# Kernel optimization log

Measured on AMD Instinct MI355X. Metric: run time of the kernel, lower is better.

Reference implementation:

```python
import jax, jax.numpy as jnp
import numpy as np
from jax import lax

VOX_DIMS = (9, 9, 9)
VOX = 9 * 9 * 9  # 729 voxels per sample


def setup_inputs() -> dict:
    rng = np.random.default_rng(0)
    N, B = 1_000_000, 32
    Cin, Fd, Cout = 3, 64, 64
    # per-point voxel index in the flat batched grid [0, B*VOX)
    voxel = rng.integers(0, B * VOX, size=N)
    unique, inverse = np.unique(voxel, return_inverse=True)

    key = jax.random.key(0)
    ks = jax.random.split(key, 12)
    s = 0.1
    inp = {
        "x": jax.random.normal(ks[0], (N, Cin), jnp.float32),
        "lin0_w": jax.random.normal(ks[1], (Cin, Fd), jnp.float32) * s,
        "lin0_b": jax.random.normal(ks[2], (Fd,), jnp.float32) * s,
        "conv0_w": jax.random.normal(ks[3], (Fd, Cin, 3, 3, 3), jnp.float32) * s,
        "conv0_b": jax.random.normal(ks[4], (Fd,), jnp.float32) * s,
        "lin1_w": jax.random.normal(ks[5], (Fd, Cout), jnp.float32) * s,
        "lin1_b": jax.random.normal(ks[6], (Cout,), jnp.float32) * s,
        "conv1_w": jax.random.normal(ks[7], (Cout, Fd, 3, 3, 3), jnp.float32) * s,
        "conv1_b": jax.random.normal(ks[8], (Cout,), jnp.float32) * s,
        "linf_w": jax.random.normal(ks[9], (Cin, Cout), jnp.float32) * s,
        "linf_b": jax.random.normal(ks[10], (Cout,), jnp.float32) * s,
        "consecutive_cluster": jnp.asarray(inverse, jnp.int32),
        "cluster_non_consecutive": jnp.asarray(voxel, jnp.int32),
        "unique_cluster_non_consecutive": jnp.asarray(unique, jnp.int32),
        "batch_size": B,
    }
    return inp


def _elm(x, lin_w, lin_b, conv_w, conv_b, consec, cnc, unc, B):
    """One EquivariantLinearMapsModule forward (use_attention is forced False)."""
    Cin = x.shape[1]
    Cout = lin_w.shape[1]
    inner = x @ lin_w + lin_b  # [N, Cout]

    U = unc.shape[0]
    sums = jax.ops.segment_sum(x, consec, num_segments=U)           # [U, Cin]
    counts = jax.ops.segment_sum(jnp.ones((x.shape[0], 1), x.dtype), consec, num_segments=U)
    means = sums / counts                                           # scatter_mean

    # grid[:, unique] = means.T ; then raw view to (B, Cin, 9, 9, 9) as in torch
    grid = jnp.zeros((Cin, B * VOX), x.dtype).at[:, unc].set(means.T)
    grid = grid.reshape((B, Cin) + VOX_DIMS)
    out = lax.conv_general_dilated(
        grid, conv_w, window_strides=(1, 1, 1), padding=[(1, 1)] * 3,
        dimension_numbers=("NCDHW", "OIDHW", "NCDHW"))
    out = out + conv_b[None, :, None, None, None]
    # raw view back to (Cout, B*VOX) then gather per point
    outer = out.reshape(Cout, -1)[:, cnc].T  # [N, Cout]
    return inner + outer


def reference(x, lin0_w, lin0_b, conv0_w, conv0_b, lin1_w, lin1_b, conv1_w, conv1_b,
              linf_w, linf_b, consecutive_cluster, cluster_non_consecutive,
              unique_cluster_non_consecutive, batch_size):
    x0 = x
    h = _elm(x0, lin0_w, lin0_b, conv0_w, conv0_b,
             consecutive_cluster, cluster_non_consecutive,
             unique_cluster_non_consecutive, batch_size)
    h = _elm(h, lin1_w, lin1_b, conv1_w, conv1_b,
             consecutive_cluster, cluster_non_consecutive,
             unique_cluster_non_consecutive, batch_size)
    # input_nc (3) < output_nc (64): residual via lin_first
    return h + (x0 @ linf_w + linf_b)
```

## Files before the change

### kernel.cpp

```cpp
#include <hip/hip_runtime.h>
#include <hip/hip_bf16.h>
#include <stdint.h>

typedef __hip_bfloat16 bf16;
typedef _Float16 half_t;
typedef _Float16 half8 __attribute__((ext_vector_type(8)));
typedef float f32x4 __attribute__((ext_vector_type(4)));
typedef unsigned short us8 __attribute__((ext_vector_type(8)));

#define BVOXN 23328

__device__ __forceinline__ float b2f(bf16 v) { return __bfloat162float(v); }

#define OFF_L0W   64
#define OFF_B0    256
#define OFF_W0    320
#define OFF_CB0   5504
#define OFF_CB1   120320
#define OFF_SUMS  120640
#define OFF_GA0   213952
#define OFF_MEX   283936
#define OFF_GT    377248
#define OFF_C0T   1123744
#define OFF_WT    1870240
#define OFF_WC    1927584
#define OFF_BVEC  1927776
#define OFF_G     1927840

#define FP_SCALE 1048576.0f
#define FP_BIAS  8388608

__global__ void k_probe(const void* lin1_w, int* flag) {
    __shared__ int cnt[256];
    int t = threadIdx.x;
    const bf16* p = (const bf16*)lin1_w;
    int c = 0;
    for (int j = t; j < 2048; j += 256) {
        float v = b2f(p[2 * j]);
        if (!(v == v) || fabsf(v) > 64.0f || (v != 0.0f && fabsf(v) < 1e-20f)) c++;
    }
    cnt[t] = c;
    __syncthreads();
    for (int s = 128; s > 0; s >>= 1) {
        if (t < s) cnt[t] += cnt[t + s];
        __syncthreads();
    }
    if (t == 0) *flag = (cnt[0] > 100) ? 1 : 0;
}

__device__ __forceinline__ float ldf(const void* p, int j, int isf) {
    return isf ? ((const float*)p)[j] : b2f(((const bf16*)p)[j]);
}

#define SETUP_N 120256
__global__ void k_sa(const void* x, const int* consec, int N, int NA,
                     const void* l0w, const void* l0b, const void* w0,
                     const void* cb0, const void* l1w, const void* l1b,
                     const void* w1, const void* cb1, const void* lfw,
                     const void* lfb, const int* flag, float* ws,
                     half_t* Wt, float* Wc, float* bvec,
                     unsigned long long* sums8) {
    int isf = *flag;
    int bid = blockIdx.x;
    if (bid < NA) {
        int i = bid * 256 + threadIdx.x;
        if (i >= N) return;
        int u = consec[i];
        float v0 = ldf(x, 3 * i + 0, isf);
        float v1 = ldf(x, 3 * i + 1, isf);
        float v2 = ldf(x, 3 * i + 2, isf);
        unsigned e0 = (unsigned)(__float2int_rn(v0 * FP_SCALE) + FP_BIAS);
        unsigned e1 = (unsigned)(__float2int_rn(v1 * FP_SCALE) + FP_BIAS);
        unsigned e2 = (unsigned)(__float2int_rn(v2 * FP_SCALE) + FP_BIAS);
        atomicAdd(&sums8[2 * u + 0], ((unsigned long long)e0 << 32) | e1);
        atomicAdd(&sums8[2 * u + 1], (1ull << 32) | e2);
        return;
    }
    int t = (bid - NA) * 256 + threadIdx.x;
    if (t < SETUP_N) {
        if (t < 5568) {
            const void* src;
            int j;
            float* dst;
            if (t < 192)       { src = l0w; j = t;         dst = ws + OFF_L0W + j; }
            else if (t < 256)  { src = l0b; j = t - 192;   dst = ws + 256 + (j = t - 192, j); }
            else if (t < 5440) {
                j = t - 256;
                int o = j / 81, r = j % 81, i = r / 27, tap = r % 27;
                src = w0;
                dst = ws + OFF_W0 + (i * 27 + tap) * 64 + o;
            }
            else if (t < 5504) { src = cb0; j = t - 5440;  dst = ws + OFF_CB0 + j; }
            else               { src = cb1; j = t - 5504;  dst = ws + OFF_CB1 + j; }
            if (t >= 192 && t < 256) { src = l0b; j = t - 192; dst = ws + OFF_B0 + j; }
            *dst = ldf(src, j, isf);
        } else {
            int q = t - 5568;
            int tap = q >> 12;
            int r = q & 4095;
            int o = r >> 6, i = r & 63;
            float v;
            if (tap < 27) v = ldf(w1, (o * 64 + i) * 27 + tap, isf);
            else          v = ldf(l1w, i * 64 + o, isf);
            Wt[q] = (half_t)v;
        }
        return;
    }
    if (bid == NA + (SETUP_N + 255) / 256 && threadIdx.x < 64) {
        int c = threadIdx.x;
        float bv = ldf(l1b, c, isf) + ldf(lfb, c, isf);
        for (int k = 0; k < 64; ++k)
            bv += ldf(l0b, k, isf) * ldf(l1w, k * 64 + c, isf);
        bvec[c] = bv;
        for (int r = 0; r < 3; ++r) {
            float wv = ldf(lfw, r * 64 + c, isf);
            for (int k = 0; k < 64; ++k)
                wv += ldf(l0w, r * 64 + k, isf) * ldf(l1w, k * 64 + c, isf);
            Wc[r * 64 + c] = wv;
        }
    }
}

__device__ __forceinline__ void decode_mean(const unsigned long long* sums8, int u,
                                            float& m0, float& m1, float& m2) {
    unsigned long long S1 = sums8[2 * u + 0];
    unsigned long long S2 = sums8[2 * u + 1];
    double n = (double)(unsigned)(S2 >> 32);
    double k = 1.0 / (1048576.0 * n);
    double nb = n * 8388608.0;
    m0 = (float)(((double)(unsigned)(S1 >> 32) - nb) * k);
    m1 = (float)(((double)(unsigned)(S1 & 0xffffffffu) - nb) * k);
    m2 = (float)(((double)(unsigned)(S2 & 0xffffffffu) - nb) * k);
}

__global__ void k_scatter0(const unsigned long long* sums8, const int* unc,
                           float* gridA0, f32x4* meanex, int U) {
    int u = blockIdx.x * 256 + threadIdx.x;
    if (u >= U) return;
    int v = unc[u];
    float m0, m1, m2;
    decode_mean(sums8, u, m0, m1, m2);
    gridA0[0 * BVOXN + v] = m0;
    gridA0[1 * BVOXN + v] = m1;
    gridA0[2 * BVOXN + v] = m2;
    f32x4 m = {m0, m1, m2, 1.0f};
    meanex[v] = m;
}

__global__ __launch_bounds__(256) void k_conv0s(const float* gridA0, const float* w0t,
                                                const float* cb0, half_t* conv0oT) {
    __shared__ float slab[3 * 363];
    int b = blockIdx.x / 9, d = blockIdx.x % 9;
    int t = threadIdx.x;
    for (int s = t; s < 3 * 363; s += 256) {
        int i = s / 363, rr = s % 363;
        int zz = rr / 121, p = rr % 121;
        int ph = p / 11, pw = p % 11;
        int z = d + zz - 1, hh = ph - 1, ww = pw - 1;
        float v = 0.0f;
        if ((unsigned)z < 9u && (unsigned)hh < 9u && (unsigned)ww < 9u)
            v = gridA0[b * 2187 + i * 729 + z * 81 + hh * 9 + ww];
        slab[s] = v;
    }
    __syncthreads();

    int og = t >> 5, l = t & 31;
    int hw[3], hj[3], wj[3];
    bool valid[3];
    #pragma unroll
    for (int j = 0; j < 3; ++j) {
        int q = l + 32 * j;
        valid[j] = q < 81;
        int qc = q < 81 ? q : 80;
        hw[j] = q; hj[j] = qc / 9; wj[j] = qc % 9;
    }
    float acc[8][3];
    #pragma unroll
    for (int oj = 0; oj < 8; ++oj) {
        float bv = cb0[og * 8 + oj];
        acc[oj][0] = bv; acc[oj][1] = bv; acc[oj][2] = bv;
    }

    for (int i = 0; i < 3; ++i) {
        const float* sb = slab + i * 363;
        const float* wb = w0t + (i * 27) * 64 + og * 8;
        for (int kd = 0; kd < 3; ++kd)
            for (int kh = 0; kh < 3; ++kh) {
                int ib0 = kd * 121 + (hj[0] + kh) * 11 + wj[0];
                int ib1 = kd * 121 + (hj[1] + kh) * 11 + wj[1];
                int ib2 = kd * 121 + (hj[2] + kh) * 11 + wj[2];
                #pragma unroll
                for (int kw = 0; kw < 3; ++kw) {
                    int tap = kd * 9 + kh * 3 + kw;
                    const float4* w4 = reinterpret_cast<const float4*>(wb + tap * 64);
                    float4 wA = w4[0];
                    float4 wB = w4[1];
                    float in0 = sb[ib0 + kw];
                    float in1 = sb[ib1 + kw];
                    float in2 = sb[ib2 + kw];
                    acc[0][0] += wA.x * in0; acc[0][1] += wA.x * in1; acc[0][2] += wA.x * in2;
                    acc[1][0] += wA.y * in0; acc[1][1] += wA.y * in1; acc[1][2] += wA.y * in2;
                    acc[2][0] += wA.z * in0; acc[2][1] += wA.z * in1; acc[2][2] += wA.z * in2;
                    acc[3][0] += wA.w * in0; acc[3][1] += wA.w * in1; acc[3][2] += wA.w * in2;
                    acc[4][0] += wB.x * in0; acc[4][1] += wB.x * in1; acc[4][2] += wB.x * in2;
                    acc[5][0] += wB.y * in0; acc[5][1] += wB.y * in1; acc[5][2] += wB.y * in2;
                    acc[6][0] += wB.z * in0; acc[6][1] += wB.z * in1; acc[6][2] += wB.z * in2;
                    acc[7][0] += wB.w * in0; acc[7][1] += wB.w * in1; acc[7][2] += wB.w * in2;
                }
            }
    }

    #pragma unroll
    for (int oj = 0; oj < 8; ++oj) {
        int o = og * 8 + oj;
        int kraw = 2 * b + (o >> 5);
        int bvr = o & 31;
        #pragma unroll
        for (int j = 0; j < 3; ++j)
            if (valid[j])
                conv0oT[(bvr * 729 + d * 81 + hw[j]) * 64 + kraw] =
                    (half_t)acc[oj][j];
    }
}

__global__ __launch_bounds__(256) void k_grid1(const f32x4* __restrict__ meanex,
                                               const half_t* __restrict__ conv0oT,
                                               const float* __restrict__ l0w,
                                               const float* __restrict__ l0b,
                                               half_t* __restrict__ gridTc) {
    int r = blockIdx.x * 4 + (threadIdx.x >> 6);
    int ch = threadIdx.x & 63;
    int bp = r / 729, pos = r % 729;
    int c = 2 * bp + (ch >> 5);
    int v = (ch & 31) * 729 + pos;
    f32x4 m = meanex[v];
    float val = 0.0f;
    if (m[3] != 0.0f)
        val = l0b[c] + m[0] * l0w[c] + m[1] * l0w[64 + c] + m[2] * l0w[128 + c] +
              (float)conv0oT[v * 64 + c];
    gridTc[r * 64 + ch] = (half_t)val;
}

__global__ __launch_bounds__(384) void k_conv1m(const half_t* __restrict__ gridTc,
                                                const half_t* __restrict__ Wt,
                                                const float* __restrict__ cb1,
                                                bf16* __restrict__ G) {
    __shared__ __align__(16) half_t slab[363 * 72];
    int bid = blockIdx.x;
    int nh = bid & 1;
    int t2 = bid >> 1;
    int b = t2 / 9, z = t2 % 9;
    int tid = threadIdx.x;

    for (int s = tid; s < 2904; s += 384) {
        int pos = s >> 3, ic = s & 7;
        int zz = pos / 121, rr = pos % 121;
        int ph = rr / 11, pw = rr % 11;
        int zi = z + zz - 1, yi = ph - 1, xi = pw - 1;
        half8 v;
        #pragma unroll
        for (int j = 0; j < 8; ++j) v[j] = (half_t)0.f;
        if ((unsigned)zi < 9u && (unsigned)yi < 9u && (unsigned)xi < 9u)
            v = *(const half8*)&gridTc[(b * 729 + zi * 81 + yi * 9 + xi) * 64 + ic * 8];
        *(half8*)&slab[pos * 72 + ic * 8] = v;
    }
    __syncthreads();

    int w = tid >> 6;
    int l = tid & 63;
    int m16 = l & 15, kb = l >> 4;
    int qbase = w * 16;
    int qa = qbase + m16; if (qa > 80) qa = 80;
    int ya = qa / 9, xa = qa % 9;
    int laneA = (ya * 11 + xa) * 72 + kb * 8;
    int o0 = nh * 32 + m16;
    f32x4 acc0 = {0.f, 0.f, 0.f, 0.f};
    f32x4 acc1 = {0.f, 0.f, 0.f, 0.f};

    const half_t* wbase = Wt + (o0 * 64 + kb * 8);

    #pragma unroll
    for (int kd = 0; kd < 3; ++kd)
      #pragma unroll
      for (int kh = 0; kh < 3; ++kh)
        #pragma unroll
        for (int kw = 0; kw < 3; ++kw) {
            int tap = kd * 9 + kh * 3 + kw;
            int sb = laneA + (kd * 121 + kh * 11 + kw) * 72;
            const half_t* wt = wbase + tap * 4096;
            #pragma unroll
            for (int is = 0; is < 2; ++is) {
                half8 a  = *(const half8*)&slab[sb + is * 32];
                half8 b0 = *(const half8*)&wt[is * 32];
                half8 b1 = *(const half8*)&wt[1024 + is * 32];
                acc0 = __builtin_amdgcn_mfma_f32_16x16x32_f16(a, b0, acc0, 0, 0, 0);
                acc1 = __builtin_amdgcn_mfma_f32_16x16x32_f16(a, b1, acc1, 0, 0, 0);
            }
        }

    float c0 = cb1[o0], c1 = cb1[o0 + 16];
    int cG = 2 * b + nh;
    int vb0 = m16 * 729 + z * 81;
    int vb1 = (m16 + 16) * 729 + z * 81;
    #pragma unroll
    for (int r = 0; r < 4; ++r) {
        int q = qbase + kb * 4 + r;
        if (q < 81) {
            G[(vb0 + q) * 64 + cG] = __float2bfloat16(acc0[r] + c0);
            G[(vb1 + q) * 64 + cG] = __float2bfloat16(acc1[r] + c1);
        }
    }
}

__global__ __launch_bounds__(256) void k_G2(const half_t* __restrict__ conv0oT,
                                            const half_t* __restrict__ Wt,
                                            bf16* __restrict__ G) {
    int wid = (blockIdx.x * 256 + threadIdx.x) >> 6;
    int v0 = wid * 16;
    if (v0 >= BVOXN) return;
    int l = threadIdx.x & 63;
    int m16 = l & 15, kb = l >> 4;
    const half_t* wt27 = Wt + 27 * 4096;
    f32x4 acc[4];
    #pragma unroll
    for (int ct = 0; ct < 4; ++ct) acc[ct] = {0.f, 0.f, 0.f, 0.f};
    const half_t* ap = conv0oT + (v0 + m16) * 64 + kb * 8;
    #pragma unroll
    for (int is = 0; is < 2; ++is) {
        half8 a = *(const half8*)&ap[is * 32];
        #pragma unroll
        for (int ct = 0; ct < 4; ++ct) {
            half8 bf = *(const half8*)&wt27[(ct * 16 + m16) * 64 + kb * 8 + is * 32];
            acc[ct] = __builtin_amdgcn_mfma_f32_16x16x32_f16(a, bf, acc[ct], 0, 0, 0);
        }
    }
    #pragma unroll
    for (int ct = 0; ct < 4; ++ct)
        #pragma unroll
        for (int r = 0; r < 4; ++r) {
            int v = v0 + kb * 4 + r;
            int c = ct * 16 + m16;
            int idx = v * 64 + c;
            G[idx] = __float2bfloat16(b2f(G[idx]) + acc[ct][r]);
        }
}

__device__ __forceinline__ unsigned short f2bf_raw(float f) {
    bf16 h = __float2bfloat16(f);
    unsigned short u;
    __builtin_memcpy(&u, &h, 2);
    return u;
}

__global__ __launch_bounds__(256) void k_out(const void* x, const int* cnc,
                                             const float* Wc, const float* bvec,
                                             const bf16* G, const int* flag,
                                             void* out, int N, int nthreads) {
    int isf = *flag;
    int tid = blockIdx.x * 256 + threadIdx.x;
    int lane = threadIdx.x & 63;
    int sub = lane & 7;
    int gb = lane & 56;
    int c8 = sub * 8;
    f32x4 w0a = *(const f32x4*)&Wc[c8];
    f32x4 w0b = *(const f32x4*)&Wc[c8 + 4];
    f32x4 w1a = *(const f32x4*)&Wc[64 + c8];
    f32x4 w1b = *(const f32x4*)&Wc[64 + c8 + 4];
    f32x4 w2a = *(const f32x4*)&Wc[128 + c8];
    f32x4 w2b = *(const f32x4*)&Wc[128 + c8 + 4];
    f32x4 bva = *(const f32x4*)&bvec[c8];
    f32x4 bvb = *(const f32x4*)&bvec[c8 + 4];
    long long tot = (long long)N * 8;
    for (long long t = tid; t < tot; t += nthreads) {
        int i = (int)(t >> 3);
        float xv = 0.0f;
        int cv = 0;
        if (sub < 3) xv = ldf(x, 3 * i + sub, isf);
        else if (sub == 3) cv = cnc[i];
        float x0 = __shfl(xv, gb + 0);
        float x1 = __shfl(xv, gb + 1);
        float x2 = __shfl(xv, gb + 2);
        int v = __shfl(cv, gb + 3);
        us8 g = *(const us8*)&G[(size_t)v * 64 + c8];
        f32x4 ra, rb;
        #pragma unroll
        for (int j = 0; j < 4; ++j) {
            float gfa = __uint_as_float((unsigned)g[j] << 16);
            float gfb = __uint_as_float((unsigned)g[j + 4] << 16);
            ra[j] = bva[j] + x0 * w0a[j] + x1 * w1a[j] + x2 * w2a[j] + gfa;
            rb[j] = bvb[j] + x0 * w0b[j] + x1 * w1b[j] + x2 * w2b[j] + gfb;
        }
        size_t oi = (size_t)i * 64 + c8;
        if (isf) {
            *(f32x4*)((float*)out + oi) = ra;
            *(f32x4*)((float*)out + oi + 4) = rb;
        } else {
            us8 h;
            #pragma unroll
            for (int j = 0; j < 4; ++j) {
                h[j] = f2bf_raw(ra[j]);
                h[j + 4] = f2bf_raw(rb[j]);
            }
            *(us8*)((bf16*)out + oi) = h;
        }
    }
}

extern "C" void kernel_launch(void* const* d_in, const int* in_sizes, int n_in,
                              void* d_out, int out_size, void* d_ws, size_t ws_size,
                              hipStream_t stream) {
    const void* x       = d_in[0];
    const void* lin0_w  = d_in[1];
    const void* lin0_b  = d_in[2];
    const void* conv0_w = d_in[3];
    const void* conv0_b = d_in[4];
    const void* lin1_w  = d_in[5];
    const void* lin1_b  = d_in[6];
    const void* conv1_w = d_in[7];
    const void* conv1_b = d_in[8];
    const void* linf_w  = d_in[9];
    const void* linf_b  = d_in[10];
    const int* consec   = (const int*)d_in[11];
    const int* cnc      = (const int*)d_in[12];
    const int* unc      = (const int*)d_in[13];

    int N = in_sizes[0] / 3;
    int U = in_sizes[13];

    float* ws   = (float*)d_ws;
    int*   flag = (int*)d_ws;
    unsigned long long* sums8 = (unsigned long long*)(ws + OFF_SUMS);
    float*  gridA0  = ws + OFF_GA0;
    f32x4*  meanex  = (f32x4*)(ws + OFF_MEX);
    half_t* gridTc  = (half_t*)(ws + OFF_GT);
    half_t* conv0oT = (half_t*)(ws + OFF_C0T);
    half_t* Wt      = (half_t*)(ws + OFF_WT);
    float*  Wc      = ws + OFF_WC;
    float*  bvec    = ws + OFF_BVEC;
    bf16*   G       = (bf16*)(ws + OFF_G);

    hipMemsetAsync((char*)d_ws + (size_t)OFF_SUMS * 4, 0,
                   (size_t)(OFF_GT - OFF_SUMS) * 4, stream);

    k_probe<<<1, 256, 0, stream>>>(lin1_w, flag);
    int NA = (N + 255) / 256;
    int SB = (SETUP_N + 255) / 256 + 1;
    k_sa<<<NA + SB, 256, 0, stream>>>(x, consec, N, NA,
        lin0_w, lin0_b, conv0_w, conv0_b, lin1_w, lin1_b, conv1_w, conv1_b,
        linf_w, linf_b, flag, ws, Wt, Wc, bvec, sums8);
    k_scatter0<<<(U + 255) / 256, 256, 0, stream>>>(sums8, unc, gridA0, meanex, U);
    k_conv0s<<<288, 256, 0, stream>>>(gridA0, ws + OFF_W0, ws + OFF_CB0, conv0oT);
    k_grid1<<<BVOXN / 4, 256, 0, stream>>>(meanex, conv0oT, ws + OFF_L0W,
                                           ws + OFF_B0, gridTc);
    k_conv1m<<<576, 384, 0, stream>>>(gridTc, Wt, ws + OFF_CB1, G);
    k_G2<<<(BVOXN / 16 * 64 + 255) / 256, 256, 0, stream>>>(conv0oT, Wt, G);
    long long tot8 = (long long)N * 8;
    int blocks = (int)((tot8 + 255) / 256);
    if (blocks > 2048) blocks = 2048;
    k_out<<<blocks, 256, 0, stream>>>(x, cnc, Wc, bvec, G, flag, d_out, N,
                                      blocks * 256);
}
```

Before: 526.5 us.

## Fuse grid1 and G2 kernels, vectorize atomic accumulation, share conv1 slab across halves

Merges the grid-building kernel and the linear G2 MFMA kernel into one launch, so G2 writes G first and conv1 then accumulates into it. The accumulation kernel now has each thread handle four points with vectorized loads of indices and features. conv1 uses 768-thread blocks that cover both output-channel halves, which halves the redundant slab loads. The aim is fewer launches and less redundant global traffic, at the cost of larger blocks and a read-modify-write in conv1.

```diff
diff --git a/kernel.cpp b/kernel.cpp
--- a/kernel.cpp
+++ b/kernel.cpp
@@ -6,6 +6,7 @@
 typedef _Float16 half_t;
 typedef _Float16 half8 __attribute__((ext_vector_type(8)));
 typedef float f32x4 __attribute__((ext_vector_type(4)));
+typedef unsigned short us4 __attribute__((ext_vector_type(4)));
 typedef unsigned short us8 __attribute__((ext_vector_type(8)));
 
 #define BVOXN 23328
@@ -52,6 +53,15 @@
     return isf ? ((const float*)p)[j] : b2f(((const bf16*)p)[j]);
 }
 
+__device__ __forceinline__ void do_atomics(unsigned long long* sums8, int u,
+                                           float v0, float v1, float v2) {
+    unsigned e0 = (unsigned)(__float2int_rn(v0 * FP_SCALE) + FP_BIAS);
+    unsigned e1 = (unsigned)(__float2int_rn(v1 * FP_SCALE) + FP_BIAS);
+    unsigned e2 = (unsigned)(__float2int_rn(v2 * FP_SCALE) + FP_BIAS);
+    atomicAdd(&sums8[2 * u + 0], ((unsigned long long)e0 << 32) | e1);
+    atomicAdd(&sums8[2 * u + 1], (1ull << 32) | e2);
+}
+
 #define SETUP_N 120256
 __global__ void k_sa(const void* x, const int* consec, int N, int NA,
                      const void* l0w, const void* l0b, const void* w0,
@@ -63,17 +73,42 @@
     int isf = *flag;
     int bid = blockIdx.x;
     if (bid < NA) {
-        int i = bid * 256 + threadIdx.x;
-        if (i >= N) return;
-        int u = consec[i];
-        float v0 = ldf(x, 3 * i + 0, isf);
-        float v1 = ldf(x, 3 * i + 1, isf);
-        float v2 = ldf(x, 3 * i + 2, isf);
-        unsigned e0 = (unsigned)(__float2int_rn(v0 * FP_SCALE) + FP_BIAS);
-        unsigned e1 = (unsigned)(__float2int_rn(v1 * FP_SCALE) + FP_BIAS);
-        unsigned e2 = (unsigned)(__float2int_rn(v2 * FP_SCALE) + FP_BIAS);
-        atomicAdd(&sums8[2 * u + 0], ((unsigned long long)e0 << 32) | e1);
-        atomicAdd(&sums8[2 * u + 1], (1ull << 32) | e2);
+        int i0 = (bid * 256 + threadIdx.x) * 4;
+        if (i0 >= N) return;
+        if (i0 + 3 < N) {
+            int4 uu = *(const int4*)&consec[i0];
+            float xv[12];
+            if (isf) {
+                f32x4 a = *(const f32x4*)((const float*)x + 3 * i0);
+                f32x4 b = *(const f32x4*)((const float*)x + 3 * i0 + 4);
+                f32x4 c = *(const f32x4*)((const float*)x + 3 * i0 + 8);
+                #pragma unroll
+                for (int j = 0; j < 4; ++j) {
+                    xv[j] = a[j]; xv[4 + j] = b[j]; xv[8 + j] = c[j];
+                }
+            } else {
+                us4 a = *(const us4*)((const bf16*)x + 3 * i0);
+                us4 b = *(const us4*)((const bf16*)x + 3 * i0 + 4);
+                us4 c = *(const us4*)((const bf16*)x + 3 * i0 + 8);
+                #pragma unroll
+                for (int j = 0; j < 4; ++j) {
+                    xv[j]     = __uint_as_float((unsigned)a[j] << 16);
+                    xv[4 + j] = __uint_as_float((unsigned)b[j] << 16);
+                    xv[8 + j] = __uint_as_float((unsigned)c[j] << 16);
+                }
+            }
+            do_atomics(sums8, uu.x, xv[0], xv[1], xv[2]);
+            do_atomics(sums8, uu.y, xv[3], xv[4], xv[5]);
+            do_atomics(sums8, uu.z, xv[6], xv[7], xv[8]);
+            do_atomics(sums8, uu.w, xv[9], xv[10], xv[11]);
+        } else {
+            for (int p = 0; p < 4; ++p) {
+                int i = i0 + p;
+                if (i >= N) break;
+                do_atomics(sums8, consec[i], ldf(x, 3 * i, isf),
+                           ldf(x, 3 * i + 1, isf), ldf(x, 3 * i + 2, isf));
+            }
+        }
         return;
     }
     int t = (bid - NA) * 256 + threadIdx.x;
@@ -83,7 +118,7 @@
             int j;
             float* dst;
             if (t < 192)       { src = l0w; j = t;         dst = ws + OFF_L0W + j; }
-            else if (t < 256)  { src = l0b; j = t - 192;   dst = ws + 256 + (j = t - 192, j); }
+            else if (t < 256)  { src = l0b; j = t - 192;   dst = ws + OFF_B0  + j; }
             else if (t < 5440) {
                 j = t - 256;
                 int o = j / 81, r = j % 81, i = r / 27, tap = r % 27;
@@ -92,7 +127,6 @@
             }
             else if (t < 5504) { src = cb0; j = t - 5440;  dst = ws + OFF_CB0 + j; }
             else               { src = cb1; j = t - 5504;  dst = ws + OFF_CB1 + j; }
-            if (t >= 192 && t < 256) { src = l0b; j = t - 192; dst = ws + OFF_B0 + j; }
             *dst = ldf(src, j, isf);
         } else {
             int q = t - 5568;
@@ -223,36 +257,68 @@
     }
 }
 
-__global__ __launch_bounds__(256) void k_grid1(const f32x4* __restrict__ meanex,
-                                               const half_t* __restrict__ conv0oT,
-                                               const float* __restrict__ l0w,
-                                               const float* __restrict__ l0b,
-                                               half_t* __restrict__ gridTc) {
-    int r = blockIdx.x * 4 + (threadIdx.x >> 6);
-    int ch = threadIdx.x & 63;
-    int bp = r / 729, pos = r % 729;
-    int c = 2 * bp + (ch >> 5);
-    int v = (ch & 31) * 729 + pos;
-    f32x4 m = meanex[v];
-    float val = 0.0f;
-    if (m[3] != 0.0f)
-        val = l0b[c] + m[0] * l0w[c] + m[1] * l0w[64 + c] + m[2] * l0w[128 + c] +
-              (float)conv0oT[v * 64 + c];
-    gridTc[r * 64 + ch] = (half_t)val;
-}
-
-__global__ __launch_bounds__(384) void k_conv1m(const half_t* __restrict__ gridTc,
+#define GRID1_BLKS (BVOXN / 4)
+#define G2_BLKS ((BVOXN / 16 * 64 + 255) / 256)
+__global__ __launch_bounds__(256) void k_vox(const f32x4* __restrict__ meanex,
+                                             const half_t* __restrict__ conv0oT,
+                                             const float* __restrict__ l0w,
+                                             const float* __restrict__ l0b,
+                                             const half_t* __restrict__ Wt,
+                                             half_t* __restrict__ gridTc,
+                                             bf16* __restrict__ G) {
+    if (blockIdx.x < GRID1_BLKS) {
+        int r = blockIdx.x * 4 + (threadIdx.x >> 6);
+        int ch = threadIdx.x & 63;
+        int bp = r / 729, pos = r % 729;
+        int c = 2 * bp + (ch >> 5);
+        int v = (ch & 31) * 729 + pos;
+        f32x4 m = meanex[v];
+        float val = 0.0f;
+        if (m[3] != 0.0f)
+            val = l0b[c] + m[0] * l0w[c] + m[1] * l0w[64 + c] + m[2] * l0w[128 + c] +
+                  (float)conv0oT[v * 64 + c];
+        gridTc[r * 64 + ch] = (half_t)val;
+        return;
+    }
+    int wid = ((blockIdx.x - GRID1_BLKS) * 256 + threadIdx.x) >> 6;
+    int v0 = wid * 16;
+    if (v0 >= BVOXN) return;
+    int l = threadIdx.x & 63;
+    int m16 = l & 15, kb = l >> 4;
+    const half_t* wt27 = Wt + 27 * 4096;
+    f32x4 acc[4];
+    #pragma unroll
+    for (int ct = 0; ct < 4; ++ct) acc[ct] = {0.f, 0.f, 0.f, 0.f};
+    const half_t* ap = conv0oT + (v0 + m16) * 64 + kb * 8;
+    #pragma unroll
+    for (int is = 0; is < 2; ++is) {
+        half8 a = *(const half8*)&ap[is * 32];
+        #pragma unroll
+        for (int ct = 0; ct < 4; ++ct) {
+            half8 bfr = *(const half8*)&wt27[(ct * 16 + m16) * 64 + kb * 8 + is * 32];
+            acc[ct] = __builtin_amdgcn_mfma_f32_16x16x32_f16(a, bfr, acc[ct], 0, 0, 0);
+        }
+    }
+    #pragma unroll
+    for (int ct = 0; ct < 4; ++ct)
+        #pragma unroll
+        for (int r = 0; r < 4; ++r) {
+            int v = v0 + kb * 4 + r;
+            int c = ct * 16 + m16;
+            G[v * 64 + c] = __float2bfloat16(acc[ct][r]);
+        }
+}
+
+__global__ __launch_bounds__(768) void k_conv1m(const half_t* __restrict__ gridTc,
                                                 const half_t* __restrict__ Wt,
                                                 const float* __restrict__ cb1,
                                                 bf16* __restrict__ G) {
     __shared__ __align__(16) half_t slab[363 * 72];
     int bid = blockIdx.x;
-    int nh = bid & 1;
-    int t2 = bid >> 1;
-    int b = t2 / 9, z = t2 % 9;
+    int b = bid / 9, z = bid % 9;
     int tid = threadIdx.x;
 
-    for (int s = tid; s < 2904; s += 384) {
+    for (int s = tid; s < 2904; s += 768) {
         int pos = s >> 3, ic = s & 7;
         int zz = pos / 121, rr = pos % 121;
         int ph = rr / 11, pw = rr % 11;
@@ -267,9 +333,10 @@
     __syncthreads();
 
     int w = tid >> 6;
+    int nh = w & 1;
     int l = tid & 63;
     int m16 = l & 15, kb = l >> 4;
-    int qbase = w * 16;
+    int qbase = (w >> 1) * 16;
     int qa = qbase + m16; if (qa > 80) qa = 80;
     int ya = qa / 9, xa = qa % 9;
     int laneA = (ya * 11 + xa) * 72 + kb * 8;
@@ -306,43 +373,12 @@
     for (int r = 0; r < 4; ++r) {
         int q = qbase + kb * 4 + r;
         if (q < 81) {
-            G[(vb0 + q) * 64 + cG] = __float2bfloat16(acc0[r] + c0);
-            G[(vb1 + q) * 64 + cG] = __float2bfloat16(acc1[r] + c1);
-        }
-    }
-}
-
-__global__ __launch_bounds__(256) void k_G2(const half_t* __restrict__ conv0oT,
-                                            const half_t* __restrict__ Wt,
-                                            bf16* __restrict__ G) {
-    int wid = (blockIdx.x * 256 + threadIdx.x) >> 6;
-    int v0 = wid * 16;
-    if (v0 >= BVOXN) return;
-    int l = threadIdx.x & 63;
-    int m16 = l & 15, kb = l >> 4;
-    const half_t* wt27 = Wt + 27 * 4096;
-    f32x4 acc[4];
-    #pragma unroll
-    for (int ct = 0; ct < 4; ++ct) acc[ct] = {0.f, 0.f, 0.f, 0.f};
-    const half_t* ap = conv0oT + (v0 + m16) * 64 + kb * 8;
-    #pragma unroll
-    for (int is = 0; is < 2; ++is) {
-        half8 a = *(const half8*)&ap[is * 32];
-        #pragma unroll
-        for (int ct = 0; ct < 4; ++ct) {
-            half8 bf = *(const half8*)&wt27[(ct * 16 + m16) * 64 + kb * 8 + is * 32];
-            acc[ct] = __builtin_amdgcn_mfma_f32_16x16x32_f16(a, bf, acc[ct], 0, 0, 0);
-        }
-    }
-    #pragma unroll
-    for (int ct = 0; ct < 4; ++ct)
-        #pragma unroll
-        for (int r = 0; r < 4; ++r) {
-            int v = v0 + kb * 4 + r;
-            int c = ct * 16 + m16;
-            int idx = v * 64 + c;
-            G[idx] = __float2bfloat16(b2f(G[idx]) + acc[ct][r]);
-        }
+            int i0 = (vb0 + q) * 64 + cG;
+            int i1 = (vb1 + q) * 64 + cG;
+            G[i0] = __float2bfloat16(b2f(G[i0]) + acc0[r] + c0);
+            G[i1] = __float2bfloat16(b2f(G[i1]) + acc1[r] + c1);
+        }
+    }
 }
 
 __device__ __forceinline__ unsigned short f2bf_raw(float f) {
@@ -443,17 +479,16 @@
                    (size_t)(OFF_GT - OFF_SUMS) * 4, stream);
 
     k_probe<<<1, 256, 0, stream>>>(lin1_w, flag);
-    int NA = (N + 255) / 256;
+    int NA = (N + 1023) / 1024;
     int SB = (SETUP_N + 255) / 256 + 1;
     k_sa<<<NA + SB, 256, 0, stream>>>(x, consec, N, NA,
         lin0_w, lin0_b, conv0_w, conv0_b, lin1_w, lin1_b, conv1_w, conv1_b,
         linf_w, linf_b, flag, ws, Wt, Wc, bvec, sums8);
     k_scatter0<<<(U + 255) / 256, 256, 0, stream>>>(sums8, unc, gridA0, meanex, U);
     k_conv0s<<<288, 256, 0, stream>>>(gridA0, ws + OFF_W0, ws + OFF_CB0, conv0oT);
-    k_grid1<<<BVOXN / 4, 256, 0, stream>>>(meanex, conv0oT, ws + OFF_L0W,
-                                           ws + OFF_B0, gridTc);
-    k_conv1m<<<576, 384, 0, stream>>>(gridTc, Wt, ws + OFF_CB1, G);
-    k_G2<<<(BVOXN / 16 * 64 + 255) / 256, 256, 0, stream>>>(conv0oT, Wt, G);
+    k_vox<<<GRID1_BLKS + G2_BLKS, 256, 0, stream>>>(meanex, conv0oT, ws + OFF_L0W,
+                                                    ws + OFF_B0, Wt, gridTc, G);
+    k_conv1m<<<288, 768, 0, stream>>>(gridTc, Wt, ws + OFF_CB1, G);
     long long tot8 = (long long)N * 8;
     int blocks = (int)((tot8 + 255) / 256);
     if (blocks > 2048) blocks = 2048;
```

After: 572.6 us. 1.09x slower.
